# Kernel tuning notes

Hardware: AMD Instinct MI355X
Metric: run time of the kernel (lower is better)

Reference implementation:

```python
import jax, jax.numpy as jnp
import numpy as np
from jax import lax

IN_CH = 256
OUT_CH = 256
INTER = IN_CH // 2
KERNEL = 3


def setup_inputs() -> dict:
    key = jax.random.key(0)
    ks = jax.random.split(key, 6)
    B, C, H, W = 8, IN_CH, 128, 128
    x = jax.random.normal(ks[0], (B, C, H, W), dtype=jnp.float32)
    s = 1.0 / np.sqrt(C)
    Wq = jax.random.normal(ks[1], (INTER, C), dtype=jnp.float32) * s
    Wk = jax.random.normal(ks[2], (INTER, C), dtype=jnp.float32) * s
    Wv = jax.random.normal(ks[3], (INTER, C), dtype=jnp.float32) * s
    w1d = jax.random.normal(ks[4], (KERNEL,), dtype=jnp.float32) * (1.0 / np.sqrt(KERNEL))
    Wc = jax.random.normal(ks[5], (OUT_CH, INTER, 3, 3), dtype=jnp.float32) * (1.0 / np.sqrt(INTER * 9))
    return {"x": x, "Wq": Wq, "Wk": Wk, "Wv": Wv, "w1d": w1d, "Wc": Wc}


def reference(x, Wq, Wk, Wv, w1d, Wc):
    B, C, H, W = x.shape
    inter = Wq.shape[0]
    Hs, Ws = H // 4, W // 4  # 1x1 conv, stride 4, pad 0 == spatial subsample
    xs = x[:, :, ::4, ::4]  # [B, C, Hs, Ws]
    q = jnp.einsum('oc,bchw->bohw', Wq, xs).reshape(B, inter, Hs * Ws)  # [B, inter, N]
    k = jnp.einsum('oc,bchw->bohw', Wk, xs).reshape(B, inter, Hs * Ws)
    v = jnp.einsum('oc,bchw->bohw', Wv, xs).reshape(B, inter, Hs * Ws)
    # gate = softmax(Q^T K) over last dim, shape [B, N, N]
    scores = jnp.einsum('bcn,bcm->bnm', q, k)
    gate = jax.nn.softmax(scores, axis=-1)
    # gated value: [B, inter, N] -> [B, inter, Hs, Ws]
    gv = jnp.einsum('bnm,bcm->bcn', gate, v).reshape(B, inter, Hs, Ws)
    # ECA channel gating: global avg pool -> conv1d over channel dim -> sigmoid
    ca = gv.mean(axis=(2, 3))  # [B, inter]
    ca = lax.conv_general_dilated(
        ca[:, None, :],                     # [B, 1, inter]
        w1d[None, None, :],                 # [1, 1, K]
        window_strides=(1,), padding=[((KERNEL - 1) // 2,) * 2],
        dimension_numbers=('NCH', 'OIH', 'NCH'))
    ca = jax.nn.sigmoid(ca)[:, 0, :, None, None]  # [B, inter, 1, 1]
    out = gv * ca
    out = lax.conv_general_dilated(
        out, Wc, window_strides=(1, 1), padding='SAME',
        dimension_numbers=('NCHW', 'OIHW', 'NCHW'))
    return out, gate, ca
```

## Files before the change

kernel.cpp:

```cpp
#include <hip/hip_runtime.h>
#include <math.h>

#define B_   8
#define C_   256
#define CI_  128
#define N_   1024
#define HW_  32
#define CO_  256

typedef __bf16 v8bf __attribute__((ext_vector_type(8)));
typedef float  f32x4 __attribute__((ext_vector_type(4)));
typedef unsigned short ushort_t;

__device__ __forceinline__ unsigned short f2bf_rne(float f) {
    unsigned int u = __float_as_uint(f);
    unsigned int r = u + 0x7FFF + ((u >> 16) & 1);
    return (unsigned short)(r >> 16);
}
__device__ __forceinline__ float bf2f(unsigned short h) {
    return __uint_as_float(((unsigned int)h) << 16);
}
__device__ __forceinline__ v8bf ld8(const ushort_t* p) {
    return *(const v8bf*)p;
}

__global__ __launch_bounds__(256) void prep_all_kernel(
    const float* __restrict__ x,
    const float* __restrict__ Wc,
    const float* __restrict__ Wq, const float* __restrict__ Wk,
    const float* __restrict__ Wv,
    ushort_t* __restrict__ Whi, ushort_t* __restrict__ Wlo,
    ushort_t* __restrict__ Wp_hi, ushort_t* __restrict__ Wp_lo,
    ushort_t* __restrict__ xs_hi, ushort_t* __restrict__ xs_lo,
    float* __restrict__ meanb)
{
    __shared__ ushort_t lh[32 * 72];
    __shared__ ushort_t ll[32 * 72];
    const int bx = blockIdx.x;
    const int tid = threadIdx.x;

    if (bx < 1152) {
        if (bx == 0) {
            *(float4*)&meanb[tid * 4] = make_float4(0.f, 0.f, 0.f, 0.f);
        }
        int idx = bx * 256 + tid;
        int o = idx / 1152;
        int r = idx - o * 1152;
        int ci = r / 9;
        int tap = r - ci * 9;
        float v = Wc[idx];
        unsigned short h = f2bf_rne(v);
        unsigned short l = f2bf_rne(v - bf2f(h));
        int didx = o * 1152 + tap * 128 + ci;
        Whi[didx] = h; Wlo[didx] = l;
    } else if (bx < 1536) {
        int j = (bx - 1152) * 256 + tid;
        int o = j >> 8, c = j & 255;
        float v = (o < 128) ? Wq[o * 256 + c]
                : (o < 256) ? Wk[(o - 128) * 256 + c]
                            : Wv[(o - 256) * 256 + c];
        unsigned short h = f2bf_rne(v);
        unsigned short l = f2bf_rne(v - bf2f(h));
        Wp_hi[j] = h; Wp_lo[j] = l;
    } else {
        const int bx2 = bx - 1536;
        const int cq = bx2 & 3;
        const int h  = (bx2 >> 2) & 31;
        const int b  = bx2 >> 7;
        const int w = tid & 31, cg = tid >> 5;
        const float4* xrow = (const float4*)x;
        float v[8];
        #pragma unroll
        for (int i = 0; i < 8; ++i) {
            int c = cq * 64 + i * 8 + cg;
            v[i] = xrow[(size_t)(b * C_ + c) * 4096 + h * 128 + w].x;
        }
        #pragma unroll
        for (int i = 0; i < 8; ++i) {
            int cl = i * 8 + cg;
            unsigned short hi = f2bf_rne(v[i]);
            unsigned short lo = f2bf_rne(v[i] - bf2f(hi));
            lh[w * 72 + cl] = hi;
            ll[w * 72 + cl] = lo;
        }
        __syncthreads();
        const int ww = tid >> 3, cs = tid & 7;
        size_t dst = ((size_t)(b * N_) + h * 32 + ww) * 256 + cq * 64 + cs * 8;
        *(uint4*)&xs_hi[dst] = *(uint4*)&lh[ww * 72 + cs * 8];
        *(uint4*)&xs_lo[dst] = *(uint4*)&ll[ww * 72 + cs * 8];
    }
}

__global__ __launch_bounds__(256) void proj_mfma_kernel(
    const ushort_t* __restrict__ Wp_hi, const ushort_t* __restrict__ Wp_lo,
    const ushort_t* __restrict__ xs_hi, const ushort_t* __restrict__ xs_lo,
    ushort_t* __restrict__ qt_hi, ushort_t* __restrict__ qt_lo,
    ushort_t* __restrict__ kt_hi, ushort_t* __restrict__ kt_lo,
    ushort_t* __restrict__ vB_hi, ushort_t* __restrict__ vB_lo)
{
    const int lin = blockIdx.x + 16 * (blockIdx.y + 6 * blockIdx.z);
    const int b    = lin & 7;
    const int rest = lin >> 3;
    const int n0 = (rest & 15) * 64;
    const int o0 = (rest >> 4) * 64;
    const int tid = threadIdx.x;
    const int l = tid & 63, wv = tid >> 6;
    const int wy = wv >> 1, wx = wv & 1;
    const int ln = l & 15, quad = l >> 4;

    const ushort_t* Ah_p[2]; const ushort_t* Al_p[2];
    const ushort_t* Bh_p[2]; const ushort_t* Bl_p[2];
    #pragma unroll
    for (int i = 0; i < 2; ++i) {
        size_t off = (size_t)(o0 + wy * 32 + i * 16 + ln) * 256 + quad * 8;
        Ah_p[i] = Wp_hi + off; Al_p[i] = Wp_lo + off;
    }
    #pragma unroll
    for (int j = 0; j < 2; ++j) {
        size_t off = ((size_t)(b * N_) + n0 + wx * 32 + j * 16 + ln) * 256 + quad * 8;
        Bh_p[j] = xs_hi + off; Bl_p[j] = xs_lo + off;
    }

    f32x4 acc[2][2];
    #pragma unroll
    for (int i = 0; i < 2; ++i)
        #pragma unroll
        for (int j = 0; j < 2; ++j) acc[i][j] = (f32x4){0.f,0.f,0.f,0.f};

    if (o0 < 256) {
        #pragma unroll 4
        for (int k0 = 0; k0 < 256; k0 += 32) {
            v8bf Ah[2], Al[2], Bh[2], Bl[2];
            #pragma unroll
            for (int i = 0; i < 2; ++i) { Ah[i] = ld8(Ah_p[i] + k0); Al[i] = ld8(Al_p[i] + k0); }
            #pragma unroll
            for (int j = 0; j < 2; ++j) { Bh[j] = ld8(Bh_p[j] + k0); Bl[j] = ld8(Bl_p[j] + k0); }
            __builtin_amdgcn_s_setprio(1);
            #pragma unroll
            for (int i = 0; i < 2; ++i)
                #pragma unroll
                for (int j = 0; j < 2; ++j) {
                    acc[i][j] = __builtin_amdgcn_mfma_f32_16x16x32_bf16(Ah[i], Bh[j], acc[i][j], 0, 0, 0);
                    acc[i][j] = __builtin_amdgcn_mfma_f32_16x16x32_bf16(Ah[i], Bl[j], acc[i][j], 0, 0, 0);
                    acc[i][j] = __builtin_amdgcn_mfma_f32_16x16x32_bf16(Al[i], Bh[j], acc[i][j], 0, 0, 0);
                }
            __builtin_amdgcn_s_setprio(0);
        }
        ushort_t* th = (o0 < 128) ? qt_hi : kt_hi;
        ushort_t* tl = (o0 < 128) ? qt_lo : kt_lo;
        const int ob = o0 & 127;
        #pragma unroll
        for (int i = 0; i < 2; ++i)
            #pragma unroll
            for (int j = 0; j < 2; ++j) {
                int oo = ob + wy * 32 + i * 16 + quad * 4;
                int n  = n0 + wx * 32 + j * 16 + ln;
                unsigned int h01 = 0, h23 = 0, l01 = 0, l23 = 0;
                #pragma unroll
                for (int r = 0; r < 4; ++r) {
                    float f = acc[i][j][r];
                    unsigned short hh = f2bf_rne(f);
                    unsigned short lo = f2bf_rne(f - bf2f(hh));
                    if (r < 2) { h01 |= ((unsigned)hh) << (16 * r); l01 |= ((unsigned)lo) << (16 * r); }
                    else       { h23 |= ((unsigned)hh) << (16 * (r - 2)); l23 |= ((unsigned)lo) << (16 * (r - 2)); }
                }
                size_t off = ((size_t)(b * N_) + n) * 128 + oo;
                *(uint2*)&th[off] = make_uint2(h01, h23);
                *(uint2*)&tl[off] = make_uint2(l01, l23);
            }
    } else {
        #pragma unroll 4
        for (int k0 = 0; k0 < 256; k0 += 32) {
            v8bf Ah[2], Al[2], Bh[2], Bl[2];
            #pragma unroll
            for (int i = 0; i < 2; ++i) { Ah[i] = ld8(Ah_p[i] + k0); Al[i] = ld8(Al_p[i] + k0); }
            #pragma unroll
            for (int j = 0; j < 2; ++j) { Bh[j] = ld8(Bh_p[j] + k0); Bl[j] = ld8(Bl_p[j] + k0); }
            __builtin_amdgcn_s_setprio(1);
            #pragma unroll
            for (int j = 0; j < 2; ++j)
                #pragma unroll
                for (int i = 0; i < 2; ++i) {
                    acc[j][i] = __builtin_amdgcn_mfma_f32_16x16x32_bf16(Bh[j], Ah[i], acc[j][i], 0, 0, 0);
                    acc[j][i] = __builtin_amdgcn_mfma_f32_16x16x32_bf16(Bh[j], Al[i], acc[j][i], 0, 0, 0);
                    acc[j][i] = __builtin_amdgcn_mfma_f32_16x16x32_bf16(Bl[j], Ah[i], acc[j][i], 0, 0, 0);
                }
            __builtin_amdgcn_s_setprio(0);
        }
        const int mhi = (n0 >> 5) + wx;
        #pragma unroll
        for (int j = 0; j < 2; ++j)
            #pragma unroll
            for (int i = 0; i < 2; ++i) {
                int c   = (o0 - 256) + wy * 32 + i * 16 + ln;
                int mlo = j * 16 + quad * 4;
                unsigned int h01 = 0, h23 = 0, l01 = 0, l23 = 0;
                #pragma unroll
                for (int r = 0; r < 4; ++r) {
                    float f = acc[j][i][r];
                    unsigned short hh = f2bf_rne(f);
                    unsigned short lo = f2bf_rne(f - bf2f(hh));
                    if (r < 2) { h01 |= ((unsigned)hh) << (16 * r); l01 |= ((unsigned)lo) << (16 * r); }
                    else       { h23 |= ((unsigned)hh) << (16 * (r - 2)); l23 |= ((unsigned)lo) << (16 * (r - 2)); }
                }
                size_t off = (((size_t)b * 32 + mhi) * 128 + c) * 32 + mlo;
                *(uint2*)&vB_hi[off] = make_uint2(h01, h23);
                *(uint2*)&vB_lo[off] = make_uint2(l01, l23);
            }
    }
}

__global__ __launch_bounds__(512, 2) void attn_fused_kernel(
    const ushort_t* __restrict__ qt_hi, const ushort_t* __restrict__ qt_lo,
    const ushort_t* __restrict__ kt_hi, const ushort_t* __restrict__ kt_lo,
    const ushort_t* __restrict__ vB_hi, const ushort_t* __restrict__ vB_lo,
    float* __restrict__ gate, float* __restrict__ gv, float* __restrict__ meanb)
{
    __shared__ __align__(16) char gsm[65536];
    __shared__ float redA[8][32];
    __shared__ float redB[8][32];

    const int lin = blockIdx.x + 32 * blockIdx.y;
    const int b  = lin & 7;
    const int n0 = (lin >> 3) * 32;
    const int tid = threadIdx.x;
    const int l = tid & 63, w = tid >> 6;
    const int ln = l & 15, quad = l >> 4;
    const int Mw = w * 128;

    const ushort_t* qb_h = qt_hi + ((size_t)(b * N_) + n0) * 128;
    const ushort_t* qb_l = qt_lo + ((size_t)(b * N_) + n0) * 128;
    const ushort_t* kb_h = kt_hi + (size_t)(b * N_) * 128;
    const ushort_t* kb_l = kt_lo + (size_t)(b * N_) * 128;

    f32x4 acc[2][8];
    #pragma unroll
    for (int nt = 0; nt < 2; ++nt)
        #pragma unroll
        for (int mt = 0; mt < 8; ++mt) acc[nt][mt] = (f32x4){0.f,0.f,0.f,0.f};

    #pragma unroll
    for (int c0 = 0; c0 < 128; c0 += 32) {
        v8bf Ah[2], Al[2];
        #pragma unroll
        for (int nt = 0; nt < 2; ++nt) {
            size_t aoff = (size_t)(nt * 16 + ln) * 128 + c0 + quad * 8;
            Ah[nt] = ld8(qb_h + aoff); Al[nt] = ld8(qb_l + aoff);
        }
        #pragma unroll
        for (int mt = 0; mt < 8; ++mt) {
            size_t boff = (size_t)(Mw + mt * 16 + ln) * 128 + c0 + quad * 8;
            v8bf Bh = ld8(kb_h + boff);
            v8bf Bl = ld8(kb_l + boff);
            __builtin_amdgcn_s_setprio(1);
            #pragma unroll
            for (int nt = 0; nt < 2; ++nt) {
                acc[nt][mt] = __builtin_amdgcn_mfma_f32_16x16x32_bf16(Ah[nt], Bh, acc[nt][mt], 0, 0, 0);
                acc[nt][mt] = __builtin_amdgcn_mfma_f32_16x16x32_bf16(Ah[nt], Bl, acc[nt][mt], 0, 0, 0);
                acc[nt][mt] = __builtin_amdgcn_mfma_f32_16x16x32_bf16(Al[nt], Bh, acc[nt][mt], 0, 0, 0);
            }
            __builtin_amdgcn_s_setprio(0);
        }
    }

    float rmax[2][4];
    #pragma unroll
    for (int nt = 0; nt < 2; ++nt)
        #pragma unroll
        for (int r = 0; r < 4; ++r) {
            float m = acc[nt][0][r];
            #pragma unroll
            for (int mt = 1; mt < 8; ++mt) m = fmaxf(m, acc[nt][mt][r]);
            rmax[nt][r] = m;
        }
    #pragma unroll
    for (int nt = 0; nt < 2; ++nt)
        #pragma unroll
        for (int r = 0; r < 4; ++r) {
            float m = rmax[nt][r];
            #pragma unroll
            for (int xm = 1; xm <= 8; xm <<= 1) m = fmaxf(m, __shfl_xor(m, xm, 64));
            rmax[nt][r] = m;
        }
    if (ln == 0) {
        #pragma unroll
        for (int nt = 0; nt < 2; ++nt)
            #pragma unroll
            for (int r = 0; r < 4; ++r)
                redA[w][nt * 16 + quad * 4 + r] = rmax[nt][r];
    }
    __syncthreads();
    #pragma unroll
    for (int nt = 0; nt < 2; ++nt)
        #pragma unroll
        for (int r = 0; r < 4; ++r) {
            int row = nt * 16 + quad * 4 + r;
            float m0 = fmaxf(fmaxf(redA[0][row], redA[1][row]),
                             fmaxf(redA[2][row], redA[3][row]));
            float m1 = fmaxf(fmaxf(redA[4][row], redA[5][row]),
                             fmaxf(redA[6][row], redA[7][row]));
            rmax[nt][r] = fmaxf(m0, m1);
        }

    float rsum[2][4];
    #pragma unroll
    for (int nt = 0; nt < 2; ++nt)
        #pragma unroll
        for (int r = 0; r < 4; ++r) {
            float s = 0.f;
            #pragma unroll
            for (int mt = 0; mt < 8; ++mt) {
                float e = __expf(acc[nt][mt][r] - rmax[nt][r]);
                acc[nt][mt][r] = e;
                s += e;
            }
            rsum[nt][r] = s;
        }
    #pragma unroll
    for (int nt = 0; nt < 2; ++nt)
        #pragma unroll
        for (int r = 0; r < 4; ++r) {
            float s = rsum[nt][r];
            #pragma unroll
            for (int xm = 1; xm <= 8; xm <<= 1) s += __shfl_xor(s, xm, 64);
            rsum[nt][r] = s;
        }
    if (ln == 0) {
        #pragma unroll
        for (int nt = 0; nt < 2; ++nt)
            #pragma unroll
            for (int r = 0; r < 4; ++r)
                redB[w][nt * 16 + quad * 4 + r] = rsum[nt][r];
    }
    __syncthreads();
    #pragma unroll
    for (int nt = 0; nt < 2; ++nt)
        #pragma unroll
        for (int r = 0; r < 4; ++r) {
            int row = nt * 16 + quad * 4 + r;
            float inv = 1.0f / ((redB[0][row] + redB[1][row] + redB[2][row] + redB[3][row]) +
                                (redB[4][row] + redB[5][row] + redB[6][row] + redB[7][row]));
            #pragma unroll
            for (int mt = 0; mt < 8; ++mt) acc[nt][mt][r] *= inv;
        }

    #pragma unroll
    for (int nt = 0; nt < 2; ++nt)
        #pragma unroll
        for (int r = 0; r < 4; ++r) {
            int nl = nt * 16 + quad * 4 + r;
            #pragma unroll
            for (int mt = 0; mt < 8; ++mt) {
                int m = Mw + mt * 16 + ln;
                int chunk = m >> 3;
                int addr = nl * 2048 + (((chunk ^ (nl & 7))) << 4) + ((m & 7) << 1);
                *(ushort_t*)&gsm[addr] = f2bf_rne(acc[nt][mt][r]);
            }
        }
    __syncthreads();

    const ushort_t* vb_h = vB_hi + (size_t)b * CI_ * N_;
    const ushort_t* vb_l = vB_lo + (size_t)b * CI_ * N_;

    f32x4 acc2[2];
    acc2[0] = (f32x4){0.f,0.f,0.f,0.f};
    acc2[1] = (f32x4){0.f,0.f,0.f,0.f};

    #pragma unroll 4
    for (int m0 = 0; m0 < 1024; m0 += 32) {
        v8bf Bg[2];
        #pragma unroll
        for (int nt = 0; nt < 2; ++nt) {
            int nl = nt * 16 + ln;
            int chunk = (m0 >> 3) + quad;
            Bg[nt] = *(const v8bf*)&gsm[nl * 2048 + (((chunk ^ (nl & 7))) << 4)];
        }
        int c = w * 16 + ln;
        size_t aoff = (((size_t)(m0 >> 5)) * 128 + c) * 32 + quad * 8;
        v8bf Avh = ld8(vb_h + aoff);
        v8bf Avl = ld8(vb_l + aoff);
        __builtin_amdgcn_s_setprio(1);
        #pragma unroll
        for (int nt = 0; nt < 2; ++nt) {
            acc2[nt] = __builtin_amdgcn_mfma_f32_16x16x32_bf16(Avh, Bg[nt], acc2[nt], 0, 0, 0);
            acc2[nt] = __builtin_amdgcn_mfma_f32_16x16x32_bf16(Avl, Bg[nt], acc2[nt], 0, 0, 0);
        }
        __builtin_amdgcn_s_setprio(0);
    }

    #pragma unroll
    for (int nt = 0; nt < 2; ++nt) {
        int n = n0 + nt * 16 + ln;
        float4 o4 = make_float4(acc2[nt][0], acc2[nt][1], acc2[nt][2], acc2[nt][3]);
        *(float4*)&gv[((size_t)(b * N_) + n) * CI_ + w * 16 + quad * 4] = o4;
    }

    float* grow = gate + (size_t)b * N_ * N_;
    #pragma unroll
    for (int nt = 0; nt < 2; ++nt)
        #pragma unroll
        for (int r = 0; r < 4; ++r) {
            int n = n0 + nt * 16 + quad * 4 + r;
            #pragma unroll
            for (int mt = 0; mt < 8; ++mt) {
                int m = Mw + mt * 16 + ln;
                grow[(size_t)n * N_ + m] = acc[nt][mt][r];
            }
        }

    float s0 = acc2[0][0] + acc2[1][0];
    float s1 = acc2[0][1] + acc2[1][1];
    float s2 = acc2[0][2] + acc2[1][2];
    float s3 = acc2[0][3] + acc2[1][3];
    #pragma unroll
    for (int xm = 1; xm <= 8; xm <<= 1) {
        s0 += __shfl_xor(s0, xm, 64);
        s1 += __shfl_xor(s1, xm, 64);
        s2 += __shfl_xor(s2, xm, 64);
        s3 += __shfl_xor(s3, xm, 64);
    }
    if (ln == 0) {
        int cb = b * CI_ + w * 16 + quad * 4;
        atomicAdd(&meanb[cb + 0], s0);
        atomicAdd(&meanb[cb + 1], s1);
        atomicAdd(&meanb[cb + 2], s2);
        atomicAdd(&meanb[cb + 3], s3);
    }
}

__global__ __launch_bounds__(256) void gvca_prep_kernel(
    const float* __restrict__ gv, const float* __restrict__ meanb,
    const float* __restrict__ w1d,
    ushort_t* __restrict__ gvh, ushort_t* __restrict__ gvl,
    float* __restrict__ ca_out)
{
    __shared__ float ca_s[128];
    const int lin = blockIdx.x;
    const int b  = lin & 7;
    const int ns = lin >> 3;
    const int tid = threadIdx.x;

    if (tid < 128) {
        const float sc = 1.0f / 1024.0f;
        int t = b * 128 + tid;
        float left  = (tid > 0)   ? meanb[t - 1] * sc : 0.0f;
        float mid   = meanb[t] * sc;
        float right = (tid < 127) ? meanb[t + 1] * sc : 0.0f;
        float val = w1d[0] * left + w1d[1] * mid + w1d[2] * right;
        float s = 1.0f / (1.0f + __expf(-val));
        ca_s[tid] = s;
        if (ns == 0) ca_out[t] = s;
    }
    __syncthreads();

    const int cl = (tid & 31) * 4;
    const int nr = tid >> 5;
    #pragma unroll
    for (int i = 0; i < 4; ++i) {
        int n = ns * 32 + nr + i * 8;
        size_t off = ((size_t)(b * N_) + n) * 128 + cl;
        float4 v4 = *(const float4*)&gv[off];
        float vv[4] = { v4.x * ca_s[cl], v4.y * ca_s[cl + 1],
                        v4.z * ca_s[cl + 2], v4.w * ca_s[cl + 3] };
        unsigned int h01 = 0, h23 = 0, l01 = 0, l23 = 0;
        #pragma unroll
        for (int t = 0; t < 4; ++t) {
            unsigned short h = f2bf_rne(vv[t]);
            unsigned short lo = f2bf_rne(vv[t] - bf2f(h));
            if (t < 2) { h01 |= ((unsigned)h) << (16 * t); l01 |= ((unsigned)lo) << (16 * t); }
            else       { h23 |= ((unsigned)h) << (16 * (t - 2)); l23 |= ((unsigned)lo) << (16 * (t - 2)); }
        }
        *(uint2*)&gvh[off] = make_uint2(h01, h23);
        *(uint2*)&gvl[off] = make_uint2(l01, l23);
    }
}

#define CV_BHI  0
#define CV_BLO  26112
__global__ __launch_bounds__(512, 1) void conv_mfma_kernel(
    const ushort_t* __restrict__ gvh, const ushort_t* __restrict__ gvl,
    const ushort_t* __restrict__ Whi, const ushort_t* __restrict__ Wlo,
    float* __restrict__ out)
{
    extern __shared__ __align__(16) char smem[];
    const int AH[2] = {52224, 68608};
    const int AL[2] = {60416, 76800};

    const int lin = blockIdx.x;
    const int b    = lin & 7;
    const int rest = lin >> 3;
    const int o0 = (rest & 3) * 64;
    const int h0 = (rest >> 2) * 4;
    const int tid = threadIdx.x;
    const int l   = tid & 63;
    const int wv  = tid >> 6;
    const int wy  = wv >> 2;
    const int wx  = wv & 3;
    const int ln  = l & 15;
    const int quad = l >> 4;

    f32x4 acc[2][2];
    #pragma unroll
    for (int i = 0; i < 2; ++i)
        #pragma unroll
        for (int j = 0; j < 2; ++j)
            acc[i][j] = (f32x4){0.f, 0.f, 0.f, 0.f};

    const int srow = tid >> 3, scol = tid & 7;
    const int la   = srow * 128 + scol * 16;
    const int csrc = scol ^ (srow & 7);

    for (int half = 0; half < 2; ++half) {
        __syncthreads();
        for (int u = tid; u < 204 * 8; u += 512) {
            int p  = u >> 3;
            int cs = u & 7;
            int hrel = p / 34;
            int c    = p - hrel * 34;
            int gr = h0 + hrel - 1;
            int gc = c - 1;
            bool ok = ((unsigned)gr < 32u) && ((unsigned)gc < 32u);
            uint4 h4 = make_uint4(0, 0, 0, 0), l4 = make_uint4(0, 0, 0, 0);
            if (ok) {
                size_t src = ((size_t)(b * N_) + gr * 32 + gc) * 128 + half * 64 + cs * 8;
                h4 = *(const uint4*)&gvh[src];
                l4 = *(const uint4*)&gvl[src];
            }
            int addr = p * 128 + ((cs ^ (p & 7)) << 4);
            *(uint4*)&smem[CV_BHI + addr] = h4;
            *(uint4*)&smem[CV_BLO + addr] = l4;
        }
        {
            size_t g = (size_t)(o0 + srow) * 1152 + half * 64 + csrc * 8;
            *(uint4*)&smem[AH[0] + la] = *(const uint4*)&Whi[g];
            *(uint4*)&smem[AL[0] + la] = *(const uint4*)&Wlo[g];
        }

        for (int tap = 0; tap < 9; ++tap) {
            __syncthreads();
            uint4 nh, nl;
            if (tap < 8) {
                size_t g = (size_t)(o0 + srow) * 1152 + (tap + 1) * 128 + half * 64 + csrc * 8;
                nh = *(const uint4*)&Whi[g];
                nl = *(const uint4*)&Wlo[g];
            }
            const int ah = AH[tap & 1], al = AL[tap & 1];
            const int dy = tap / 3, dx = tap - dy * 3;
            const int pbase = (wx + dy) * 34 + dx;
            #pragma unroll
            for (int cc = 0; cc < 2; ++cc) {
                v8bf Bh[2], Bl[2], Ah2[2], Al2[2];
                #pragma unroll
                for (int j = 0; j < 2; ++j) {
                    int p = pbase + j * 16 + ln;
                    int ch = cc * 4 + quad;
                    int addr = p * 128 + ((ch ^ (p & 7)) << 4);
                    Bh[j] = *(const v8bf*)&smem[CV_BHI + addr];
                    Bl[j] = *(const v8bf*)&smem[CV_BLO + addr];
                }
                #pragma unroll
                for (int i = 0; i < 2; ++i) {
                    int o = wy * 32 + i * 16 + ln;
                    int ch = cc * 4 + quad;
                    int addr = o * 128 + ((ch ^ (o & 7)) << 4);
                    Ah2[i] = *(const v8bf*)&smem[ah + addr];
                    Al2[i] = *(const v8bf*)&smem[al + addr];
                }
                __builtin_amdgcn_s_setprio(1);
                #pragma unroll
                for (int i = 0; i < 2; ++i)
                    #pragma unroll
                    for (int j = 0; j < 2; ++j) {
                        acc[i][j] = __builtin_amdgcn_mfma_f32_16x16x32_bf16(Ah2[i], Bh[j], acc[i][j], 0, 0, 0);
                        acc[i][j] = __builtin_amdgcn_mfma_f32_16x16x32_bf16(Ah2[i], Bl[j], acc[i][j], 0, 0, 0);
                        acc[i][j] = __builtin_amdgcn_mfma_f32_16x16x32_bf16(Al2[i], Bh[j], acc[i][j], 0, 0, 0);
                    }
                __builtin_amdgcn_s_setprio(0);
            }
            if (tap < 8) {
                int nb = (tap + 1) & 1;
                *(uint4*)&smem[AH[nb] + la] = nh;
                *(uint4*)&smem[AL[nb] + la] = nl;
            }
        }
    }

    const int h = h0 + wx;
    #pragma unroll
    for (int i = 0; i < 2; ++i)
        #pragma unroll
        for (int j = 0; j < 2; ++j)
            #pragma unroll
            for (int r = 0; r < 4; ++r) {
                int o = o0 + wy * 32 + i * 16 + quad * 4 + r;
                int w = j * 16 + ln;
                out[(size_t)(b * CO_ + o) * N_ + h * 32 + w] = acc[i][j][r];
            }
}

extern "C" void kernel_launch(void* const* d_in, const int* in_sizes, int n_in,
                              void* d_out, int out_size, void* d_ws, size_t ws_size,
                              hipStream_t stream) {
    const float* x   = (const float*)d_in[0];
    const float* Wq  = (const float*)d_in[1];
    const float* Wk  = (const float*)d_in[2];
    const float* Wv  = (const float*)d_in[3];
    const float* w1d = (const float*)d_in[4];
    const float* Wc  = (const float*)d_in[5];

    float* out  = (float*)d_out;
    float* gate = out + 2097152;
    float* ca   = gate + 8388608;

    float*    gv      = (float*)d_ws;
    float*    meanb   = gv + 1048576;
    ushort_t* Whi     = (ushort_t*)(meanb + 1024);
    ushort_t* Wlo     = Whi + 294912;
    ushort_t* Wp_hi   = Wlo + 294912;
    ushort_t* Wp_lo   = Wp_hi + 98304;
    ushort_t* xs_hi   = Wp_lo + 98304;
    ushort_t* xs_lo   = xs_hi + 2097152;
    ushort_t* qt_hi   = xs_lo + 2097152;
    ushort_t* qt_lo   = qt_hi + 1048576;
    ushort_t* kt_hi   = qt_lo + 1048576;
    ushort_t* kt_lo   = kt_hi + 1048576;
    ushort_t* vB_hi   = kt_lo + 1048576;
    ushort_t* vB_lo   = vB_hi + 1048576;
    ushort_t* gvh     = vB_lo + 1048576;
    ushort_t* gvl     = gvh + 1048576;

    static bool s_attr_done = false;
    if (!s_attr_done) {
        hipFuncSetAttribute((const void*)conv_mfma_kernel,
                            hipFuncAttributeMaxDynamicSharedMemorySize, 84992);
        s_attr_done = true;
    }

    prep_all_kernel<<<dim3(2560), 256, 0, stream>>>(
        x, Wc, Wq, Wk, Wv, Whi, Wlo, Wp_hi, Wp_lo, xs_hi, xs_lo, meanb);
    proj_mfma_kernel<<<dim3(16, 6, 8), 256, 0, stream>>>(
        Wp_hi, Wp_lo, xs_hi, xs_lo, qt_hi, qt_lo, kt_hi, kt_lo, vB_hi, vB_lo);
    attn_fused_kernel<<<dim3(32, 8), 512, 0, stream>>>(
        qt_hi, qt_lo, kt_hi, kt_lo, vB_hi, vB_lo, gate, gv, meanb);
    gvca_prep_kernel<<<dim3(256), 256, 0, stream>>>(
        gv, meanb, w1d, gvh, gvl, ca);
    conv_mfma_kernel<<<dim3(256), 512, 84992, stream>>>(
        gvh, gvl, Whi, Wlo, out);
}
```

Baseline: 276.5 us.

## Fuse input subsample and bf16 split into QKV projection kernel via LDS

Moves the stride-4 subsampling and hi/lo bf16 split of x out of the prep kernel and into the projection kernel. Each block stages its 32 spatial positions times 256 channels in swizzled shared memory and computes all 384 Q/K/V output channels. This removes the xs_hi/xs_lo global round trip and one stage of work. In exchange, each block reloads the full projection weights from global memory, and the grid shrinks to 256 blocks with more accumulators per wave, which may lower occupancy.

```diff
diff --git a/kernel.cpp b/kernel.cpp
--- a/kernel.cpp
+++ b/kernel.cpp
@@ -25,17 +25,13 @@
 }
 
 __global__ __launch_bounds__(256) void prep_all_kernel(
-    const float* __restrict__ x,
     const float* __restrict__ Wc,
     const float* __restrict__ Wq, const float* __restrict__ Wk,
     const float* __restrict__ Wv,
     ushort_t* __restrict__ Whi, ushort_t* __restrict__ Wlo,
     ushort_t* __restrict__ Wp_hi, ushort_t* __restrict__ Wp_lo,
-    ushort_t* __restrict__ xs_hi, ushort_t* __restrict__ xs_lo,
     float* __restrict__ meanb)
 {
-    __shared__ ushort_t lh[32 * 72];
-    __shared__ ushort_t ll[32 * 72];
     const int bx = blockIdx.x;
     const int tid = threadIdx.x;
 
@@ -53,7 +49,7 @@
         unsigned short l = f2bf_rne(v - bf2f(h));
         int didx = o * 1152 + tap * 128 + ci;
         Whi[didx] = h; Wlo[didx] = l;
-    } else if (bx < 1536) {
+    } else {
         int j = (bx - 1152) * 256 + tid;
         int o = j >> 8, c = j & 255;
         float v = (o < 128) ? Wq[o * 256 + c]
@@ -62,151 +58,140 @@
         unsigned short h = f2bf_rne(v);
         unsigned short l = f2bf_rne(v - bf2f(h));
         Wp_hi[j] = h; Wp_lo[j] = l;
-    } else {
-        const int bx2 = bx - 1536;
-        const int cq = bx2 & 3;
-        const int h  = (bx2 >> 2) & 31;
-        const int b  = bx2 >> 7;
-        const int w = tid & 31, cg = tid >> 5;
-        const float4* xrow = (const float4*)x;
-        float v[8];
-        #pragma unroll
-        for (int i = 0; i < 8; ++i) {
-            int c = cq * 64 + i * 8 + cg;
-            v[i] = xrow[(size_t)(b * C_ + c) * 4096 + h * 128 + w].x;
-        }
-        #pragma unroll
-        for (int i = 0; i < 8; ++i) {
-            int cl = i * 8 + cg;
-            unsigned short hi = f2bf_rne(v[i]);
-            unsigned short lo = f2bf_rne(v[i] - bf2f(hi));
-            lh[w * 72 + cl] = hi;
-            ll[w * 72 + cl] = lo;
-        }
-        __syncthreads();
-        const int ww = tid >> 3, cs = tid & 7;
-        size_t dst = ((size_t)(b * N_) + h * 32 + ww) * 256 + cq * 64 + cs * 8;
-        *(uint4*)&xs_hi[dst] = *(uint4*)&lh[ww * 72 + cs * 8];
-        *(uint4*)&xs_lo[dst] = *(uint4*)&ll[ww * 72 + cs * 8];
-    }
-}
-
-__global__ __launch_bounds__(256) void proj_mfma_kernel(
+    }
+}
+
+__global__ __launch_bounds__(256) void proj_fused_kernel(
+    const float* __restrict__ x,
     const ushort_t* __restrict__ Wp_hi, const ushort_t* __restrict__ Wp_lo,
-    const ushort_t* __restrict__ xs_hi, const ushort_t* __restrict__ xs_lo,
     ushort_t* __restrict__ qt_hi, ushort_t* __restrict__ qt_lo,
     ushort_t* __restrict__ kt_hi, ushort_t* __restrict__ kt_lo,
     ushort_t* __restrict__ vB_hi, ushort_t* __restrict__ vB_lo)
 {
-    const int lin = blockIdx.x + 16 * (blockIdx.y + 6 * blockIdx.z);
-    const int b    = lin & 7;
-    const int rest = lin >> 3;
-    const int n0 = (rest & 15) * 64;
-    const int o0 = (rest >> 4) * 64;
+    __shared__ __align__(16) char xsm[32768];
+    const int lin = blockIdx.x;
+    const int b  = lin & 7;
+    const int n5 = lin >> 3;
+    const int n0 = n5 * 32;
     const int tid = threadIdx.x;
+
+    {
+        const int w = tid & 31, cg = tid >> 5;
+        #pragma unroll
+        for (int j = 0; j < 4; ++j) {
+            const int cbase = j * 64 + cg * 8;
+            float v[8];
+            #pragma unroll
+            for (int i = 0; i < 8; ++i)
+                v[i] = x[((size_t)(b * C_ + cbase + i) * 128 + n5 * 4) * 128 + w * 4];
+            unsigned int hw[4], lw[4];
+            #pragma unroll
+            for (int p = 0; p < 4; ++p) {
+                unsigned short h0 = f2bf_rne(v[2 * p]);
+                unsigned short l0 = f2bf_rne(v[2 * p] - bf2f(h0));
+                unsigned short h1 = f2bf_rne(v[2 * p + 1]);
+                unsigned short l1 = f2bf_rne(v[2 * p + 1] - bf2f(h1));
+                hw[p] = (unsigned)h0 | ((unsigned)h1 << 16);
+                lw[p] = (unsigned)l0 | ((unsigned)l1 << 16);
+            }
+            const int chunk = j * 8 + cg;
+            const int addr = w * 512 + ((chunk ^ (w & 7)) << 4);
+            *(uint4*)&xsm[addr]         = make_uint4(hw[0], hw[1], hw[2], hw[3]);
+            *(uint4*)&xsm[16384 + addr] = make_uint4(lw[0], lw[1], lw[2], lw[3]);
+        }
+    }
+    __syncthreads();
+
     const int l = tid & 63, wv = tid >> 6;
-    const int wy = wv >> 1, wx = wv & 1;
     const int ln = l & 15, quad = l >> 4;
 
-    const ushort_t* Ah_p[2]; const ushort_t* Al_p[2];
-    const ushort_t* Bh_p[2]; const ushort_t* Bl_p[2];
-    #pragma unroll
-    for (int i = 0; i < 2; ++i) {
-        size_t off = (size_t)(o0 + wy * 32 + i * 16 + ln) * 256 + quad * 8;
-        Ah_p[i] = Wp_hi + off; Al_p[i] = Wp_lo + off;
-    }
-    #pragma unroll
-    for (int j = 0; j < 2; ++j) {
-        size_t off = ((size_t)(b * N_) + n0 + wx * 32 + j * 16 + ln) * 256 + quad * 8;
-        Bh_p[j] = xs_hi + off; Bl_p[j] = xs_lo + off;
-    }
-
-    f32x4 acc[2][2];
-    #pragma unroll
-    for (int i = 0; i < 2; ++i)
-        #pragma unroll
-        for (int j = 0; j < 2; ++j) acc[i][j] = (f32x4){0.f,0.f,0.f,0.f};
-
-    if (o0 < 256) {
-        #pragma unroll 4
-        for (int k0 = 0; k0 < 256; k0 += 32) {
-            v8bf Ah[2], Al[2], Bh[2], Bl[2];
-            #pragma unroll
-            for (int i = 0; i < 2; ++i) { Ah[i] = ld8(Ah_p[i] + k0); Al[i] = ld8(Al_p[i] + k0); }
-            #pragma unroll
-            for (int j = 0; j < 2; ++j) { Bh[j] = ld8(Bh_p[j] + k0); Bl[j] = ld8(Bl_p[j] + k0); }
-            __builtin_amdgcn_s_setprio(1);
-            #pragma unroll
-            for (int i = 0; i < 2; ++i)
-                #pragma unroll
-                for (int j = 0; j < 2; ++j) {
-                    acc[i][j] = __builtin_amdgcn_mfma_f32_16x16x32_bf16(Ah[i], Bh[j], acc[i][j], 0, 0, 0);
-                    acc[i][j] = __builtin_amdgcn_mfma_f32_16x16x32_bf16(Ah[i], Bl[j], acc[i][j], 0, 0, 0);
-                    acc[i][j] = __builtin_amdgcn_mfma_f32_16x16x32_bf16(Al[i], Bh[j], acc[i][j], 0, 0, 0);
-                }
-            __builtin_amdgcn_s_setprio(0);
-        }
-        ushort_t* th = (o0 < 128) ? qt_hi : kt_hi;
-        ushort_t* tl = (o0 < 128) ? qt_lo : kt_lo;
-        const int ob = o0 & 127;
-        #pragma unroll
-        for (int i = 0; i < 2; ++i)
+    f32x4 acc[6][2];
+    #pragma unroll
+    for (int t = 0; t < 6; ++t)
+        #pragma unroll
+        for (int j = 0; j < 2; ++j) acc[t][j] = (f32x4){0.f,0.f,0.f,0.f};
+
+    #pragma unroll 2
+    for (int k0 = 0; k0 < 256; k0 += 32) {
+        v8bf Bh[2], Bl[2];
+        #pragma unroll
+        for (int j = 0; j < 2; ++j) {
+            int row = j * 16 + ln;
+            int chunk = (k0 >> 3) + quad;
+            int addr = row * 512 + ((chunk ^ (row & 7)) << 4);
+            Bh[j] = *(const v8bf*)&xsm[addr];
+            Bl[j] = *(const v8bf*)&xsm[16384 + addr];
+        }
+        v8bf Ah[6], Al[6];
+        #pragma unroll
+        for (int t = 0; t < 6; ++t) {
+            int st = wv + 4 * t;
+            size_t off = (size_t)(st * 16 + ln) * 256 + k0 + quad * 8;
+            Ah[t] = ld8(Wp_hi + off); Al[t] = ld8(Wp_lo + off);
+        }
+        __builtin_amdgcn_s_setprio(1);
+        #pragma unroll
+        for (int t = 0; t < 4; ++t)
             #pragma unroll
             for (int j = 0; j < 2; ++j) {
-                int oo = ob + wy * 32 + i * 16 + quad * 4;
-                int n  = n0 + wx * 32 + j * 16 + ln;
-                unsigned int h01 = 0, h23 = 0, l01 = 0, l23 = 0;
-                #pragma unroll
-                for (int r = 0; r < 4; ++r) {
-                    float f = acc[i][j][r];
-                    unsigned short hh = f2bf_rne(f);
-                    unsigned short lo = f2bf_rne(f - bf2f(hh));
-                    if (r < 2) { h01 |= ((unsigned)hh) << (16 * r); l01 |= ((unsigned)lo) << (16 * r); }
-                    else       { h23 |= ((unsigned)hh) << (16 * (r - 2)); l23 |= ((unsigned)lo) << (16 * (r - 2)); }
-                }
-                size_t off = ((size_t)(b * N_) + n) * 128 + oo;
-                *(uint2*)&th[off] = make_uint2(h01, h23);
-                *(uint2*)&tl[off] = make_uint2(l01, l23);
-            }
-    } else {
-        #pragma unroll 4
-        for (int k0 = 0; k0 < 256; k0 += 32) {
-            v8bf Ah[2], Al[2], Bh[2], Bl[2];
-            #pragma unroll
-            for (int i = 0; i < 2; ++i) { Ah[i] = ld8(Ah_p[i] + k0); Al[i] = ld8(Al_p[i] + k0); }
-            #pragma unroll
-            for (int j = 0; j < 2; ++j) { Bh[j] = ld8(Bh_p[j] + k0); Bl[j] = ld8(Bl_p[j] + k0); }
-            __builtin_amdgcn_s_setprio(1);
-            #pragma unroll
-            for (int j = 0; j < 2; ++j)
-                #pragma unroll
-                for (int i = 0; i < 2; ++i) {
-                    acc[j][i] = __builtin_amdgcn_mfma_f32_16x16x32_bf16(Bh[j], Ah[i], acc[j][i], 0, 0, 0);
-                    acc[j][i] = __builtin_amdgcn_mfma_f32_16x16x32_bf16(Bh[j], Al[i], acc[j][i], 0, 0, 0);
-                    acc[j][i] = __builtin_amdgcn_mfma_f32_16x16x32_bf16(Bl[j], Ah[i], acc[j][i], 0, 0, 0);
-                }
-            __builtin_amdgcn_s_setprio(0);
-        }
-        const int mhi = (n0 >> 5) + wx;
-        #pragma unroll
-        for (int j = 0; j < 2; ++j)
-            #pragma unroll
-            for (int i = 0; i < 2; ++i) {
-                int c   = (o0 - 256) + wy * 32 + i * 16 + ln;
-                int mlo = j * 16 + quad * 4;
-                unsigned int h01 = 0, h23 = 0, l01 = 0, l23 = 0;
-                #pragma unroll
-                for (int r = 0; r < 4; ++r) {
-                    float f = acc[j][i][r];
-                    unsigned short hh = f2bf_rne(f);
-                    unsigned short lo = f2bf_rne(f - bf2f(hh));
-                    if (r < 2) { h01 |= ((unsigned)hh) << (16 * r); l01 |= ((unsigned)lo) << (16 * r); }
-                    else       { h23 |= ((unsigned)hh) << (16 * (r - 2)); l23 |= ((unsigned)lo) << (16 * (r - 2)); }
-                }
-                size_t off = (((size_t)b * 32 + mhi) * 128 + c) * 32 + mlo;
-                *(uint2*)&vB_hi[off] = make_uint2(h01, h23);
-                *(uint2*)&vB_lo[off] = make_uint2(l01, l23);
-            }
+                acc[t][j] = __builtin_amdgcn_mfma_f32_16x16x32_bf16(Ah[t], Bh[j], acc[t][j], 0, 0, 0);
+                acc[t][j] = __builtin_amdgcn_mfma_f32_16x16x32_bf16(Ah[t], Bl[j], acc[t][j], 0, 0, 0);
+                acc[t][j] = __builtin_amdgcn_mfma_f32_16x16x32_bf16(Al[t], Bh[j], acc[t][j], 0, 0, 0);
+            }
+        #pragma unroll
+        for (int t = 4; t < 6; ++t)
+            #pragma unroll
+            for (int j = 0; j < 2; ++j) {
+                acc[t][j] = __builtin_amdgcn_mfma_f32_16x16x32_bf16(Bh[j], Ah[t], acc[t][j], 0, 0, 0);
+                acc[t][j] = __builtin_amdgcn_mfma_f32_16x16x32_bf16(Bh[j], Al[t], acc[t][j], 0, 0, 0);
+                acc[t][j] = __builtin_amdgcn_mfma_f32_16x16x32_bf16(Bl[j], Ah[t], acc[t][j], 0, 0, 0);
+            }
+        __builtin_amdgcn_s_setprio(0);
+    }
+
+    #pragma unroll
+    for (int t = 0; t < 4; ++t) {
+        const int st = wv + 4 * t;
+        ushort_t* th = (t < 2) ? qt_hi : kt_hi;
+        ushort_t* tl = (t < 2) ? qt_lo : kt_lo;
+        const int oo = (st & 7) * 16 + quad * 4;
+        #pragma unroll
+        for (int j = 0; j < 2; ++j) {
+            int n = n0 + j * 16 + ln;
+            unsigned int h01 = 0, h23 = 0, l01 = 0, l23 = 0;
+            #pragma unroll
+            for (int r = 0; r < 4; ++r) {
+                float f = acc[t][j][r];
+                unsigned short hh = f2bf_rne(f);
+                unsigned short lo = f2bf_rne(f - bf2f(hh));
+                if (r < 2) { h01 |= ((unsigned)hh) << (16 * r); l01 |= ((unsigned)lo) << (16 * r); }
+                else       { h23 |= ((unsigned)hh) << (16 * (r - 2)); l23 |= ((unsigned)lo) << (16 * (r - 2)); }
+            }
+            size_t off = ((size_t)(b * N_) + n) * 128 + oo;
+            *(uint2*)&th[off] = make_uint2(h01, h23);
+            *(uint2*)&tl[off] = make_uint2(l01, l23);
+        }
+    }
+    #pragma unroll
+    for (int t = 4; t < 6; ++t) {
+        const int st = wv + 4 * t;
+        const int c = (st - 16) * 16 + ln;
+        #pragma unroll
+        for (int j = 0; j < 2; ++j) {
+            int mlo = j * 16 + quad * 4;
+            unsigned int h01 = 0, h23 = 0, l01 = 0, l23 = 0;
+            #pragma unroll
+            for (int r = 0; r < 4; ++r) {
+                float f = acc[t][j][r];
+                unsigned short hh = f2bf_rne(f);
+                unsigned short lo = f2bf_rne(f - bf2f(hh));
+                if (r < 2) { h01 |= ((unsigned)hh) << (16 * r); l01 |= ((unsigned)lo) << (16 * r); }
+                else       { h23 |= ((unsigned)hh) << (16 * (r - 2)); l23 |= ((unsigned)lo) << (16 * (r - 2)); }
+            }
+            size_t off = (((size_t)b * 32 + n5) * 128 + c) * 32 + mlo;
+            *(uint2*)&vB_hi[off] = make_uint2(h01, h23);
+            *(uint2*)&vB_lo[off] = make_uint2(l01, l23);
+        }
     }
 }
 
@@ -618,9 +603,7 @@
     ushort_t* Wlo     = Whi + 294912;
     ushort_t* Wp_hi   = Wlo + 294912;
     ushort_t* Wp_lo   = Wp_hi + 98304;
-    ushort_t* xs_hi   = Wp_lo + 98304;
-    ushort_t* xs_lo   = xs_hi + 2097152;
-    ushort_t* qt_hi   = xs_lo + 2097152;
+    ushort_t* qt_hi   = Wp_lo + 98304;
     ushort_t* qt_lo   = qt_hi + 1048576;
     ushort_t* kt_hi   = qt_lo + 1048576;
     ushort_t* kt_lo   = kt_hi + 1048576;
@@ -636,10 +619,10 @@
         s_attr_done = true;
     }
 
-    prep_all_kernel<<<dim3(2560), 256, 0, stream>>>(
-        x, Wc, Wq, Wk, Wv, Whi, Wlo, Wp_hi, Wp_lo, xs_hi, xs_lo, meanb);
-    proj_mfma_kernel<<<dim3(16, 6, 8), 256, 0, stream>>>(
-        Wp_hi, Wp_lo, xs_hi, xs_lo, qt_hi, qt_lo, kt_hi, kt_lo, vB_hi, vB_lo);
+    prep_all_kernel<<<dim3(1536), 256, 0, stream>>>(
+        Wc, Wq, Wk, Wv, Whi, Wlo, Wp_hi, Wp_lo, meanb);
+    proj_fused_kernel<<<dim3(256), 256, 0, stream>>>(
+        x, Wp_hi, Wp_lo, qt_hi, qt_lo, kt_hi, kt_lo, vB_hi, vB_lo);
     attn_fused_kernel<<<dim3(32, 8), 512, 0, stream>>>(
         qt_hi, qt_lo, kt_hi, kt_lo, vB_hi, vB_lo, gate, gv, meanb);
     gvca_prep_kernel<<<dim3(256), 256, 0, stream>>>(
```

Measured after the change: 265.1 us. 1.04x faster.
